# Optimization experiments

Measured on AMD Instinct MI355X. Metric: run time of the kernel, lower is better.

Reference implementation:

```python
import jax, jax.numpy as jnp
import numpy as np

B, S, D = 64, 4096, 512


def setup_inputs() -> dict:
    key = jax.random.key(0)
    k1, k2, k3 = jax.random.split(key, 3)
    topic_embedding = jax.random.normal(k1, (B, D), dtype=jnp.float32)
    sequence_embedding = jax.random.normal(k2, (B, S, D), dtype=jnp.float32)
    # tfr Bilinear(D, D, output_dim=1): score = emb1^T W emb2 + bias
    W = jax.random.normal(k3, (D, D), dtype=jnp.float32) / np.sqrt(D)
    bias = jnp.zeros((1,), dtype=jnp.float32)
    return {"topic_embedding": topic_embedding,
            "sequence_embedding": sequence_embedding,
            "W": W, "bias": bias}


def reference(topic_embedding, sequence_embedding, W, bias):
    # Original: repeat topic over seq dim, map_fn over batch applying
    # bilinear(topic, token) then softmax over tokens. Vectorized:
    # factor the bilinear form: score[b,s] = (topic[b] @ W) . seq[b,s] + bias
    t = topic_embedding @ W                                  # [B, D]
    scores = jnp.einsum('bd,bsd->bs', t, sequence_embedding) + bias  # [B, S]
    beta = jax.nn.softmax(scores, axis=-1)                   # [B, S]
    return beta
```

## Files before the change

kernel.cpp:

```cpp
#include <hip/hip_runtime.h>
#include <math.h>

#define BB 64
#define SS 4096
#define DD 512

__global__ __launch_bounds__(256) void tW_kernel(const float* __restrict__ topic,
                                                 const float* __restrict__ W,
                                                 float* __restrict__ t) {
    __shared__ float tp[DD];
    __shared__ float4 part[256];
    const int b      = blockIdx.x >> 2;
    const int dchunk = (blockIdx.x & 3) * 32;
    const int dg     = threadIdx.x & 31;
    const int strip  = threadIdx.x >> 5;
    for (int i = threadIdx.x; i < DD; i += 256) tp[i] = topic[b * DD + i];
    __syncthreads();
    const float4* W4 = (const float4*)W;
    float4 acc = {0.f, 0.f, 0.f, 0.f};
    const int k0 = strip * 64;
#pragma unroll 8
    for (int k = 0; k < 64; ++k) {
        const float s  = tp[k0 + k];
        const float4 w = W4[(size_t)(k0 + k) * 128 + dchunk + dg];
        acc.x += s * w.x; acc.y += s * w.y; acc.z += s * w.z; acc.w += s * w.w;
    }
    part[threadIdx.x] = acc;
    __syncthreads();
    if (threadIdx.x < 32) {
        float4 r = part[threadIdx.x];
#pragma unroll
        for (int st = 1; st < 8; ++st) {
            const float4 q = part[st * 32 + threadIdx.x];
            r.x += q.x; r.y += q.y; r.z += q.z; r.w += q.w;
        }
        ((float4*)(t + b * DD))[dchunk + dg] = r;
    }
}

__global__ __launch_bounds__(256) void scores_kernel(const float* __restrict__ t,
                                                     const float* __restrict__ seq,
                                                     const float* __restrict__ bias,
                                                     float* __restrict__ scores) {
    const int b    = blockIdx.y;
    const int s0   = blockIdx.x << 5;
    const int wave = threadIdx.x >> 6;
    const int lane = threadIdx.x & 63;

    const float4* trow = (const float4*)(t + b * DD);
    const float4 ta = trow[lane];
    const float4 tb = trow[lane + 64];
    const float bs = bias[0];

    const float4* base = (const float4*)(seq + ((size_t)b * SS + s0) * DD);
    float* srow = scores + (size_t)b * SS + s0;

#pragma unroll
    for (int j = 0; j < 8; j += 2) {
        const int i0 = wave + 4 * j;
        const int i1 = i0 + 4;
        const float4* p0 = base + (size_t)i0 * 128;
        const float4* p1 = base + (size_t)i1 * 128;
        const float4 a0 = p0[lane], c0 = p0[lane + 64];
        const float4 a1 = p1[lane], c1 = p1[lane + 64];
        float r0 = a0.x * ta.x + a0.y * ta.y + a0.z * ta.z + a0.w * ta.w
                 + c0.x * tb.x + c0.y * tb.y + c0.z * tb.z + c0.w * tb.w;
        float r1 = a1.x * ta.x + a1.y * ta.y + a1.z * ta.z + a1.w * ta.w
                 + c1.x * tb.x + c1.y * tb.y + c1.z * tb.z + c1.w * tb.w;
#pragma unroll
        for (int m = 32; m; m >>= 1) {
            r0 += __shfl_xor(r0, m, 64);
            r1 += __shfl_xor(r1, m, 64);
        }
        if (lane == 0) {
            srow[i0] = r0 + bs;
            srow[i1] = r1 + bs;
        }
    }
}

__global__ __launch_bounds__(1024) void softmax_kernel(const float* __restrict__ scores,
                                                       float* __restrict__ out) {
    __shared__ float red[16];
    const int b   = blockIdx.x;
    const int tid = threadIdx.x;
    const int wave = tid >> 6, lane = tid & 63;

    const float4 v = ((const float4*)(scores + (size_t)b * SS))[tid];

    float m = fmaxf(fmaxf(v.x, v.y), fmaxf(v.z, v.w));
#pragma unroll
    for (int k = 32; k; k >>= 1) m = fmaxf(m, __shfl_xor(m, k, 64));
    if (lane == 0) red[wave] = m;
    __syncthreads();
    if (tid < 16) {
        float x = red[tid];
#pragma unroll
        for (int k = 8; k; k >>= 1) x = fmaxf(x, __shfl_xor(x, k, 16));
        if (tid == 0) red[0] = x;
    }
    __syncthreads();
    m = red[0];
    __syncthreads();

    float4 e;
    e.x = __expf(v.x - m); e.y = __expf(v.y - m);
    e.z = __expf(v.z - m); e.w = __expf(v.w - m);
    float s = e.x + e.y + e.z + e.w;
#pragma unroll
    for (int k = 32; k; k >>= 1) s += __shfl_xor(s, k, 64);
    if (lane == 0) red[wave] = s;
    __syncthreads();
    if (tid < 16) {
        float x = red[tid];
#pragma unroll
        for (int k = 8; k; k >>= 1) x += __shfl_xor(x, k, 16);
        if (tid == 0) red[0] = x;
    }
    __syncthreads();
    const float inv = 1.f / red[0];

    float4 o;
    o.x = e.x * inv; o.y = e.y * inv; o.z = e.z * inv; o.w = e.w * inv;
    ((float4*)(out + (size_t)b * SS))[tid] = o;
}

extern "C" void kernel_launch(void* const* d_in, const int* in_sizes, int n_in,
                              void* d_out, int out_size, void* d_ws, size_t ws_size,
                              hipStream_t stream) {
    const float* topic = (const float*)d_in[0];
    const float* seq   = (const float*)d_in[1];
    const float* W     = (const float*)d_in[2];
    const float* bias  = (const float*)d_in[3];
    float* out = (float*)d_out;

    float* t      = (float*)d_ws;
    float* scores = t + BB * DD;

    tW_kernel<<<dim3(BB * 4), 256, 0, stream>>>(topic, W, t);
    scores_kernel<<<dim3(SS / 32, BB), 256, 0, stream>>>(t, seq, bias, scores);
    softmax_kernel<<<dim3(BB), 1024, 0, stream>>>(scores, out);
}
```

Measured before the change: 684.2 us.

## Stage sequence tiles through LDS with register prefetch in scores kernel

The scores kernel now has each block handle 64 rows. Column chunks of the sequence are loaded into registers, written to a padded shared-memory tile, and the next chunk is prefetched while the current one is reduced. Each row's dot product is split across 4 threads with a short shuffle reduction, replacing the full 64-lane wave reduction per row. This trades the wave-wide shuffle reductions for extra LDS traffic and barriers on a purely bandwidth-bound streaming pass, and it uses more shared memory per block.

```diff
diff --git a/kernel.cpp b/kernel.cpp
--- a/kernel.cpp
+++ b/kernel.cpp
@@ -38,45 +38,57 @@
     }
 }
 
+#define ROWS 64
+#define F4R  128
+#define LSTR 33
 __global__ __launch_bounds__(256) void scores_kernel(const float* __restrict__ t,
                                                      const float* __restrict__ seq,
                                                      const float* __restrict__ bias,
                                                      float* __restrict__ scores) {
-    const int b    = blockIdx.y;
-    const int s0   = blockIdx.x << 5;
-    const int wave = threadIdx.x >> 6;
-    const int lane = threadIdx.x & 63;
+    __shared__ float4 tile[ROWS * LSTR];
+    __shared__ float4 tvec4[DD / 4];
+    const int b   = blockIdx.y;
+    const int s0  = blockIdx.x * ROWS;
+    const int tid = threadIdx.x;
+    const int row  = tid >> 2;
+    const int part = tid & 3;
 
-    const float4* trow = (const float4*)(t + b * DD);
-    const float4 ta = trow[lane];
-    const float4 tb = trow[lane + 64];
-    const float bs = bias[0];
+    for (int i = tid; i < DD / 4; i += 256)
+        tvec4[i] = ((const float4*)(t + (size_t)b * DD))[i];
 
     const float4* base = (const float4*)(seq + ((size_t)b * SS + s0) * DD);
-    float* srow = scores + (size_t)b * SS + s0;
+    const int r0 = tid >> 5;
+    const int g  = tid & 31;
 
+    float4 rv[8];
 #pragma unroll
-    for (int j = 0; j < 8; j += 2) {
-        const int i0 = wave + 4 * j;
-        const int i1 = i0 + 4;
-        const float4* p0 = base + (size_t)i0 * 128;
-        const float4* p1 = base + (size_t)i1 * 128;
-        const float4 a0 = p0[lane], c0 = p0[lane + 64];
-        const float4 a1 = p1[lane], c1 = p1[lane + 64];
-        float r0 = a0.x * ta.x + a0.y * ta.y + a0.z * ta.z + a0.w * ta.w
-                 + c0.x * tb.x + c0.y * tb.y + c0.z * tb.z + c0.w * tb.w;
-        float r1 = a1.x * ta.x + a1.y * ta.y + a1.z * ta.z + a1.w * ta.w
-                 + c1.x * tb.x + c1.y * tb.y + c1.z * tb.z + c1.w * tb.w;
+    for (int u = 0; u < 8; ++u)
+        rv[u] = base[(size_t)(r0 + 8 * u) * F4R + g];
+
+    float acc = 0.f;
 #pragma unroll
-        for (int m = 32; m; m >>= 1) {
-            r0 += __shfl_xor(r0, m, 64);
-            r1 += __shfl_xor(r1, m, 64);
+    for (int c = 0; c < 4; ++c) {
+        __syncthreads();
+#pragma unroll
+        for (int u = 0; u < 8; ++u)
+            tile[(r0 + 8 * u) * LSTR + g] = rv[u];
+        __syncthreads();
+        if (c < 3) {
+#pragma unroll
+            for (int u = 0; u < 8; ++u)
+                rv[u] = base[(size_t)(r0 + 8 * u) * F4R + (c + 1) * 32 + g];
         }
-        if (lane == 0) {
-            srow[i0] = r0 + bs;
-            srow[i1] = r1 + bs;
+#pragma unroll
+        for (int k = 0; k < 8; ++k) {
+            const float4 v  = tile[row * LSTR + part * 8 + k];
+            const float4 tv = tvec4[c * 32 + part * 8 + k];
+            acc += v.x * tv.x + v.y * tv.y + v.z * tv.z + v.w * tv.w;
         }
     }
+    acc += __shfl_xor(acc, 1, 64);
+    acc += __shfl_xor(acc, 2, 64);
+    if (part == 0)
+        scores[(size_t)b * SS + s0 + row] = acc + bias[0];
 }
 
 __global__ __launch_bounds__(1024) void softmax_kernel(const float* __restrict__ scores,
@@ -138,6 +150,6 @@
     float* scores = t + BB * DD;
 
     tW_kernel<<<dim3(BB * 4), 256, 0, stream>>>(topic, W, t);
-    scores_kernel<<<dim3(SS / 32, BB), 256, 0, stream>>>(t, seq, bias, scores);
+    scores_kernel<<<dim3(SS / ROWS, BB), 256, 0, stream>>>(t, seq, bias, scores);
     softmax_kernel<<<dim3(BB), 1024, 0, stream>>>(scores, out);
 }
```

Measured after the change: 756.2 us. 1.11x slower.
